# Kernel optimization log

Hardware: AMD Instinct MI355X
Metric: run time of the kernel (lower is better)

Reference implementation:

```python
import jax, jax.numpy as jnp
import numpy as np

EPS = 1e-5
DILATIONS = (1, 2, 4)


def conv2d(x, w, b, pad, groups=1, dil=1):
    # x [B,C,H,W], w [O, C//groups, kh, kw]
    y = jax.lax.conv_general_dilated(
        x, w, window_strides=(1, 1),
        padding=[(pad[0], pad[0]), (pad[1], pad[1])],
        rhs_dilation=(dil, dil),
        dimension_numbers=('NCHW', 'OIHW', 'NCHW'),
        feature_group_count=groups)
    return y + b[None, :, None, None]


def bn(x, p):
    # inference BatchNorm2d; p rows = gamma, beta, mean, var
    g, b, m, v = p[0], p[1], p[2], p[3]
    scale = g * jax.lax.rsqrt(v + EPS)
    return x * scale[None, :, None, None] + (b - m * scale)[None, :, None, None]


def bilinear_sample(img, yy, xx):
    # img [C,H,W]; yy,xx [K,H,W] float sampling coords; zero outside -> [C,K,H,W]
    H, W = img.shape[1], img.shape[2]
    y0f = jnp.floor(yy); x0f = jnp.floor(xx)
    wy1 = yy - y0f; wy0 = 1.0 - wy1
    wx1 = xx - x0f; wx0 = 1.0 - wx1

    def gather(yi, xi):
        valid = (yi >= 0) & (yi < H) & (xi >= 0) & (xi < W)
        yc = jnp.clip(yi, 0, H - 1).astype(jnp.int32)
        xc = jnp.clip(xi, 0, W - 1).astype(jnp.int32)
        v = img[:, yc, xc]  # [C,K,H,W]
        return v * valid.astype(img.dtype)

    y1f = y0f + 1.0; x1f = x0f + 1.0
    return (gather(y0f, x0f) * (wy0 * wx0) + gather(y0f, x1f) * (wy0 * wx1)
            + gather(y1f, x0f) * (wy1 * wx0) + gather(y1f, x1f) * (wy1 * wx1))


def deform_depthwise(x, off, weight, dil):
    # torchvision DeformConv2d, groups=C, kernel 3x3, stride 1, pad=dil, no bias.
    # x [B,C,H,W], off [B,18,H,W] (per-kernel-point (dy,dx)), weight [C,3,3]
    B, C, H, W = x.shape
    off = off.reshape(B, 9, 2, H, W)
    hh = jnp.arange(H, dtype=x.dtype)[:, None]
    ww = jnp.arange(W, dtype=x.dtype)[None, :]
    k = jnp.arange(3, dtype=x.dtype) - 1.0
    ky = jnp.repeat(k, 3)  # [9] row offsets
    kx = jnp.tile(k, 3)    # [9] col offsets
    w9 = weight.reshape(C, 9)

    def per_batch(xb, offb):
        yy = offb[:, 0] + hh[None] + (ky * dil)[:, None, None]  # [9,H,W]
        xx = offb[:, 1] + ww[None] + (kx * dil)[:, None, None]
        s = bilinear_sample(xb, yy, xx)  # [C,9,H,W]
        return jnp.einsum('ckhw,ck->chw', s, w9)

    return jax.vmap(per_batch)(x, off)


def setup_inputs() -> dict:
    key = jax.random.key(0)
    ks = jax.random.split(key, 20)
    B, C, H, W = 2, 64, 192, 192
    r = jax.random.normal
    u = lambda k, s: jax.random.uniform(k, s, minval=0.5, maxval=1.5)
    return {
        'x': r(ks[0], (B, C, H, W)),
        'w_off1': r(ks[1], (C, 1, 1, 15)) * 0.1, 'b_off1': r(ks[2], (C,)) * 0.1,
        'bn_off1': u(ks[3], (4, C)),
        'w_off2': r(ks[4], (C, 1, 15, 1)) * 0.1, 'b_off2': r(ks[5], (C,)) * 0.1,
        'bn_off2': u(ks[6], (4, C)),
        'w_off3': r(ks[7], (C, 1, 3, 3)) * 0.1, 'b_off3': r(ks[8], (C,)) * 0.1,
        'bn_off3': u(ks[9], (4, C)),
        'w_bal_off': r(ks[10], (18, C, 1, 1)) * 0.1, 'b_bal_off': r(ks[11], (18,)) * 0.1,
        'bn_bal_off': u(ks[12], (4, 18)),
        'w_def': r(ks[13], (3, C, 3, 3)) * 0.1,
        'w_bal': r(ks[14], (C, C, 1, 1)) * 0.1, 'b_bal': r(ks[15], (C,)) * 0.1,
        'bn_bal': u(ks[16], (4, C)),
    }


def reference(x, w_off1, b_off1, bn_off1, w_off2, b_off2, bn_off2,
              w_off3, b_off3, bn_off3, w_bal_off, b_bal_off, bn_bal_off,
              w_def, w_bal, b_bal, bn_bal):
    C = x.shape[1]
    # DirectionOffsets: three depthwise conv+BN branches summed, then 1x1 conv+BN -> 18ch
    off_sum = (bn(conv2d(x, w_off1, b_off1, (0, 7), groups=C), bn_off1)
               + bn(conv2d(x, w_off2, b_off2, (7, 0), groups=C), bn_off2)
               + bn(conv2d(x, w_off3, b_off3, (1, 1), groups=C), bn_off3))
    offsets = bn(conv2d(off_sum, w_bal_off, b_bal_off, (0, 0)), bn_bal_off)  # [B,18,H,W]
    # sum of depthwise deformable conv branches (shared offsets, different dilation)
    deform_sum = sum(deform_depthwise(x, offsets, w_def[i], float(d))
                     for i, d in enumerate(DILATIONS))
    # final balance (1x1 conv + BN) gated by x
    return bn(conv2d(deform_sum, w_bal, b_bal, (0, 0)), bn_bal) * x
```

## Files before the change

### kernel.cpp

```cpp
#include <hip/hip_runtime.h>
#include <stdint.h>

constexpr int B = 2, C = 64, H = 192, W = 192;
constexpr int HW = H * W;
constexpr int P = B * H * W;
constexpr float EPS = 1e-5f;

__device__ __forceinline__ int swz(int bid, int nwg) {
  return (bid & 7) * (nwg >> 3) + (bid >> 3);
}

__global__ __launch_bounds__(256) void k_prepw(const float* __restrict__ w1,
    const float* __restrict__ w2, const float* __restrict__ w3,
    const float* __restrict__ wdef, float* __restrict__ w1t,
    float* __restrict__ w2t, float* __restrict__ w3t, float* __restrict__ wdeft) {
  int gid = blockIdx.x * 256 + threadIdx.x;
  const int stride = 8 * 256;
  for (int i = gid; i < 960; i += stride) {
    int c = i & 63, j = i >> 6;
    w1t[i] = w1[c * 15 + j];
    w2t[i] = w2[c * 15 + j];
  }
  for (int i = gid; i < 576; i += stride) {
    int c = i & 63, j = i >> 6;
    w3t[i] = w3[c * 9 + j];
  }
  for (int i = gid; i < 1728; i += stride) {
    int c = i & 63, jk = i >> 6;
    int di = jk / 9, k = jk % 9;
    wdeft[i] = wdef[di * (C * 9) + c * 9 + k];
  }
}

__global__ __launch_bounds__(256) void k_transpose(const float* __restrict__ x,
                                                   float* __restrict__ xt) {
  int blk = swz(blockIdx.x, B * H * (W / 64));
  int wt  = blk % (W / 64);
  int h   = (blk / (W / 64)) % H;
  int b   = blk / ((W / 64) * H);
  int w0  = wt * 64;
  __shared__ float tile[64][65];
  int tx = threadIdx.x & 63;
  int ty = threadIdx.x >> 6;
  #pragma unroll
  for (int c = ty; c < 64; c += 4)
    tile[c][tx] = x[((b * C + c) * H + h) * W + w0 + tx];
  __syncthreads();
  #pragma unroll
  for (int wi = ty; wi < 64; wi += 4)
    xt[((b * H + h) * W + w0 + wi) * 64 + tx] = tile[tx][wi];
}

__global__ __launch_bounds__(256) void k_offsum(const float* __restrict__ xt,
    const float* __restrict__ w1t, const float* __restrict__ b1, const float* __restrict__ bn1,
    const float* __restrict__ w2t, const float* __restrict__ b2, const float* __restrict__ bn2,
    const float* __restrict__ w3t, const float* __restrict__ b3, const float* __restrict__ bn3,
    float* __restrict__ out) {
  int wave = (swz(blockIdx.x, P / 16) * 256 + (int)threadIdx.x) >> 6;
  int c = threadIdx.x & 63;
  int w0 = (wave % (W / 4)) * 4;
  int h  = (wave / (W / 4)) % H;
  int b  = wave / ((W / 4) * H);
  const float* xb = xt + (size_t)b * HW * 64 + c;

  float s1[4] = {0.f, 0.f, 0.f, 0.f};
  float s2[4] = {0.f, 0.f, 0.f, 0.f};
  float s3[4] = {0.f, 0.f, 0.f, 0.f};

  {
    float xv[18];
    #pragma unroll
    for (int j = 0; j < 18; ++j) {
      int ww = w0 - 7 + j;
      xv[j] = (ww >= 0 && ww < W) ? xb[(h * W + ww) * 64] : 0.f;
    }
    #pragma unroll
    for (int j = 0; j < 15; ++j) {
      float wj = w1t[j * 64 + c];
      #pragma unroll
      for (int p = 0; p < 4; ++p) s1[p] = fmaf(xv[p + j], wj, s1[p]);
    }
  }
  #pragma unroll
  for (int j = 0; j < 15; ++j) {
    int hh = h - 7 + j;
    if (hh >= 0 && hh < H) {
      float wj = w2t[j * 64 + c];
      #pragma unroll
      for (int p = 0; p < 4; ++p)
        s2[p] = fmaf(xb[(hh * W + w0 + p) * 64], wj, s2[p]);
    }
  }
  #pragma unroll
  for (int dy = -1; dy <= 1; ++dy) {
    int hh = h + dy;
    if (hh < 0 || hh >= H) continue;
    float rv[6];
    #pragma unroll
    for (int j = 0; j < 6; ++j) {
      int ww = w0 - 1 + j;
      rv[j] = (ww >= 0 && ww < W) ? xb[(hh * W + ww) * 64] : 0.f;
    }
    #pragma unroll
    for (int dx = 0; dx < 3; ++dx) {
      float wj = w3t[((dy + 1) * 3 + dx) * 64 + c];
      #pragma unroll
      for (int p = 0; p < 4; ++p) s3[p] = fmaf(rv[p + dx], wj, s3[p]);
    }
  }

  float sc1 = bn1[c] / sqrtf(bn1[192 + c] + EPS);
  float sh1 = bn1[64 + c] - bn1[128 + c] * sc1;
  float sc2 = bn2[c] / sqrtf(bn2[192 + c] + EPS);
  float sh2 = bn2[64 + c] - bn2[128 + c] * sc2;
  float sc3 = bn3[c] / sqrtf(bn3[192 + c] + EPS);
  float sh3 = bn3[64 + c] - bn3[128 + c] * sc3;
  float bb1 = b1[c], bb2 = b2[c], bb3 = b3[c];
  #pragma unroll
  for (int p = 0; p < 4; ++p)
    out[((size_t)wave * 4 + p) * 64 + c] =
        fmaf(s1[p] + bb1, sc1, sh1) + fmaf(s2[p] + bb2, sc2, sh2) +
        fmaf(s3[p] + bb3, sc3, sh3);
}

__global__ __launch_bounds__(256) void k_offsets(const float* __restrict__ off_sum,
    const float* __restrict__ wq, const float* __restrict__ bq,
    const float* __restrict__ bnq, float* __restrict__ out) {
  int idx = swz(blockIdx.x, (P * 18) / 256) * 256 + (int)threadIdx.x;
  int o   = idx % 18;
  int pix = idx / 18;
  const float4* v  = (const float4*)(off_sum + (size_t)pix * 64);
  const float4* wv = (const float4*)(wq + o * 64);
  float s = 0.f;
  #pragma unroll
  for (int j = 0; j < 16; ++j) {
    float4 a = v[j], ww = wv[j];
    s = fmaf(a.x, ww.x, s); s = fmaf(a.y, ww.y, s);
    s = fmaf(a.z, ww.z, s); s = fmaf(a.w, ww.w, s);
  }
  float sc = bnq[o] / sqrtf(bnq[54 + o] + EPS);
  float sh = bnq[18 + o] - bnq[36 + o] * sc;
  out[idx] = fmaf(s + bq[o], sc, sh);
}

__global__ __launch_bounds__(256) void k_deform(const float* __restrict__ xt,
                                                const float* __restrict__ offs,
                                                const float* __restrict__ wdeft,
                                                float* __restrict__ dsum) {
  __shared__ uint32_t lpre[4][27 * 8 + 4];
  int wl   = threadIdx.x >> 6;
  int lane = threadIdx.x & 63;
  int pix  = swz(blockIdx.x, P / 4) * 4 + wl;

  if (lane < 27) {
    int di = lane / 9, k = lane % 9;
    int d  = 1 << di;
    int w = pix % W, h = (pix / W) % H;
    float offy = offs[(size_t)pix * 18 + 2 * k];
    float offx = offs[(size_t)pix * 18 + 2 * k + 1];
    int ky = k / 3 - 1, kx = k % 3 - 1;
    float yy = (offy + (float)h) + (float)(ky * d);
    float xx = (offx + (float)w) + (float)(kx * d);
    float y0f = floorf(yy), x0f = floorf(xx);
    float wy1 = yy - y0f, wx1 = xx - x0f;
    float wy0 = 1.f - wy1, wx0 = 1.f - wx1;
    int y0 = (int)fmaxf(fminf(y0f, 1.0e4f), -1.0e4f);
    int x0 = (int)fmaxf(fminf(x0f, 1.0e4f), -1.0e4f);
    int y1 = y0 + 1, x1 = x0 + 1;
    float my0 = (y0 >= 0 && y0 < H) ? 1.f : 0.f;
    float my1 = (y1 >= 0 && y1 < H) ? 1.f : 0.f;
    float mx0 = (x0 >= 0 && x0 < W) ? 1.f : 0.f;
    float mx1 = (x1 >= 0 && x1 < W) ? 1.f : 0.f;
    int y0c = min(max(y0, 0), H - 1), y1c = min(max(y1, 0), H - 1);
    int x0c = min(max(x0, 0), W - 1), x1c = min(max(x1, 0), W - 1);
    uint32_t packed = (uint32_t)y0c | ((uint32_t)y1c << 8) |
                      ((uint32_t)x0c << 16) | ((uint32_t)x1c << 24);
    float wy0m = wy0 * my0, wy1m = wy1 * my1;
    float wx0m = wx0 * mx0, wx1m = wx1 * mx1;
    uint32_t* q = &lpre[wl][lane * 8];
    q[0] = packed;
    q[1] = __float_as_uint(wy0m * wx0m);
    q[2] = __float_as_uint(wy0m * wx1m);
    q[3] = __float_as_uint(wy1m * wx0m);
    q[4] = __float_as_uint(wy1m * wx1m);
  }
  __syncthreads();

  int c = lane;
  int b = pix / HW;
  const float* xb = xt + (size_t)b * HW * 64 + c;

  float wd[27];
  #pragma unroll
  for (int i = 0; i < 27; ++i) wd[i] = wdeft[i * 64 + c];

  float acc = 0.f;
  #pragma unroll
  for (int t = 0; t < 27; ++t) {
    uint4 m = *(const uint4*)&lpre[wl][t * 8];
    float w11 = __uint_as_float(lpre[wl][t * 8 + 4]);
    uint32_t pk = m.x;
    float w00 = __uint_as_float(m.y);
    float w01 = __uint_as_float(m.z);
    float w10 = __uint_as_float(m.w);
    int y0 = pk & 255, y1 = (pk >> 8) & 255;
    int x0 = (pk >> 16) & 255, x1 = pk >> 24;
    int r0 = y0 * W, r1 = y1 * W;
    float v00 = xb[(size_t)(r0 + x0) * 64];
    float v01 = xb[(size_t)(r0 + x1) * 64];
    float v10 = xb[(size_t)(r1 + x0) * 64];
    float v11 = xb[(size_t)(r1 + x1) * 64];
    float bil = fmaf(v11, w11, fmaf(v10, w10, fmaf(v01, w01, v00 * w00)));
    acc = fmaf(wd[t], bil, acc);
  }
  dsum[(size_t)pix * 64 + c] = acc;
}

__global__ __launch_bounds__(256) void k_final(const float* __restrict__ ds,
    const float* __restrict__ x, const float* __restrict__ wb,
    const float* __restrict__ bb, const float* __restrict__ bnb,
    float* __restrict__ out) {
  int blk = swz(blockIdx.x, P / 64);
  int w0 = (blk % (W / 64)) * 64;
  int h  = (blk / (W / 64)) % H;
  int b  = blk / ((W / 64) * H);
  __shared__ float dtile[64][68];
  __shared__ float scs[64], shb[64];
  int tx = threadIdx.x & 63;
  int ty = threadIdx.x >> 6;
  int pixbase = (b * H + h) * W + w0;

  {
    int pr  = threadIdx.x >> 4;
    int ic4 = (threadIdx.x & 15) * 4;
    #pragma unroll
    for (int pass = 0; pass < 4; ++pass) {
      int pix = pass * 16 + pr;
      float4 v = *(const float4*)&ds[(size_t)(pixbase + pix) * 64 + ic4];
      *(float4*)&dtile[pix][ic4] = v;
    }
  }
  if (threadIdx.x < 64) {
    float g = bnb[threadIdx.x], vv = bnb[192 + threadIdx.x];
    float sc = g / sqrtf(vv + EPS);
    scs[threadIdx.x] = sc;
    shb[threadIdx.x] = fmaf(bb[threadIdx.x], sc,
                            bnb[64 + threadIdx.x] - bnb[128 + threadIdx.x] * sc);
  }
  __syncthreads();

  float dreg[64];
  #pragma unroll
  for (int q = 0; q < 16; ++q) {
    float4 v = *(float4*)&dtile[tx][q * 4];
    dreg[4 * q + 0] = v.x; dreg[4 * q + 1] = v.y;
    dreg[4 * q + 2] = v.z; dreg[4 * q + 3] = v.w;
  }

  int ocb = __builtin_amdgcn_readfirstlane(ty);
  #pragma unroll
  for (int j = 0; j < 16; ++j) {
    int oc = ocb + 4 * j;
    const float* wr = wb + oc * 64;
    float a0 = 0.f, a1 = 0.f, a2 = 0.f, a3 = 0.f;
    #pragma unroll
    for (int q = 0; q < 16; ++q) {
      a0 = fmaf(dreg[4 * q + 0], wr[4 * q + 0], a0);
      a1 = fmaf(dreg[4 * q + 1], wr[4 * q + 1], a1);
      a2 = fmaf(dreg[4 * q + 2], wr[4 * q + 2], a2);
      a3 = fmaf(dreg[4 * q + 3], wr[4 * q + 3], a3);
    }
    float s = (a0 + a1) + (a2 + a3);
    float val = fmaf(s, scs[oc], shb[oc]);
    int xi = ((b * C + oc) * H + h) * W + w0 + tx;
    out[xi] = val * x[xi];
  }
}

extern "C" void kernel_launch(void* const* d_in, const int* in_sizes, int n_in,
                              void* d_out, int out_size, void* d_ws, size_t ws_size,
                              hipStream_t stream) {
  const float* x     = (const float*)d_in[0];
  const float* w1    = (const float*)d_in[1];
  const float* b1    = (const float*)d_in[2];
  const float* bn1   = (const float*)d_in[3];
  const float* w2    = (const float*)d_in[4];
  const float* b2    = (const float*)d_in[5];
  const float* bn2   = (const float*)d_in[6];
  const float* w3    = (const float*)d_in[7];
  const float* b3    = (const float*)d_in[8];
  const float* bn3   = (const float*)d_in[9];
  const float* wbo   = (const float*)d_in[10];
  const float* bbo   = (const float*)d_in[11];
  const float* bnbo  = (const float*)d_in[12];
  const float* wdef  = (const float*)d_in[13];
  const float* wbal  = (const float*)d_in[14];
  const float* bbal  = (const float*)d_in[15];
  const float* bnbal = (const float*)d_in[16];
  float* out = (float*)d_out;

  float*    xt      = (float*)d_ws;
  float*    off_sum = xt + (size_t)P * 64;
  float*    offs    = off_sum + (size_t)P * 64;
  float*    wts     = offs + (size_t)P * 18;
  float*    w1t     = wts;
  float*    w2t     = wts + 960;
  float*    w3t     = wts + 1920;
  float*    wdeft   = wts + 2496;
  float*    dsum    = off_sum;

  k_prepw<<<8, 256, 0, stream>>>(w1, w2, w3, wdef, w1t, w2t, w3t, wdeft);
  k_transpose<<<B * H * (W / 64), 256, 0, stream>>>(x, xt);
  k_offsum<<<P / 16, 256, 0, stream>>>(xt, w1t, b1, bn1, w2t, b2, bn2, w3t, b3, bn3, off_sum);
  k_offsets<<<(P * 18) / 256, 256, 0, stream>>>(off_sum, wbo, bbo, bnbo, offs);
  k_deform<<<P / 4, 256, 0, stream>>>(xt, offs, wdeft, dsum);
  k_final<<<P / 64, 256, 0, stream>>>(dsum, x, wbal, bbal, bnbal, out);
}
```

Measured before the change: 291.2 us.

## Fuse offset-sum and 1x1 offset conv; precompute byte offsets with scalar addressing in deform

Merges the depthwise offset-sum kernel and the 18-channel 1x1 offset projection into one kernel. The per-pixel 64-channel sums now stay in shared memory and the projection weights are staged there, so the off_sum intermediate is never written to or read back from global memory. In the deform kernel, the four bilinear corner addresses are precomputed as byte offsets in LDS and read with readfirstlane, which makes them wave-uniform scalar bases and removes per-lane unpacking and multiplies. The cost is a 64-float register array per thread in the fused kernel, which may lower occupancy.

```diff
diff --git a/kernel.cpp b/kernel.cpp
--- a/kernel.cpp
+++ b/kernel.cpp
@@ -51,22 +51,37 @@
     xt[((b * H + h) * W + w0 + wi) * 64 + tx] = tile[tx][wi];
 }
 
-__global__ __launch_bounds__(256) void k_offsum(const float* __restrict__ xt,
+__global__ __launch_bounds__(256) void k_offpipe(const float* __restrict__ xt,
     const float* __restrict__ w1t, const float* __restrict__ b1, const float* __restrict__ bn1,
     const float* __restrict__ w2t, const float* __restrict__ b2, const float* __restrict__ bn2,
     const float* __restrict__ w3t, const float* __restrict__ b3, const float* __restrict__ bn3,
-    float* __restrict__ out) {
-  int wave = (swz(blockIdx.x, P / 16) * 256 + (int)threadIdx.x) >> 6;
-  int c = threadIdx.x & 63;
-  int w0 = (wave % (W / 4)) * 4;
-  int h  = (wave / (W / 4)) % H;
-  int b  = wave / ((W / 4) * H);
+    const float* __restrict__ wq, const float* __restrict__ bq, const float* __restrict__ bnq,
+    float* __restrict__ offs) {
+  __shared__ float os[16][68];
+  __shared__ float wqs[18][66];
+  __shared__ float qsc[18], qsh[18];
+
+  int blk = swz(blockIdx.x, P / 16);
+  int w0t = (blk % (W / 16)) * 16;
+  int h   = (blk / (W / 16)) % H;
+  int b   = blk / ((W / 16) * H);
+  int wl  = threadIdx.x >> 6;
+  int c   = threadIdx.x & 63;
+  int w0  = w0t + wl * 4;
   const float* xb = xt + (size_t)b * HW * 64 + c;
+
+  for (int i = threadIdx.x; i < 18 * 64; i += 256)
+    wqs[i >> 6][i & 63] = wq[i];
+  if (threadIdx.x < 18) {
+    int o = threadIdx.x;
+    float sc = bnq[o] / sqrtf(bnq[54 + o] + EPS);
+    qsc[o] = sc;
+    qsh[o] = fmaf(bq[o], sc, bnq[18 + o] - bnq[36 + o] * sc);
+  }
 
   float s1[4] = {0.f, 0.f, 0.f, 0.f};
   float s2[4] = {0.f, 0.f, 0.f, 0.f};
   float s3[4] = {0.f, 0.f, 0.f, 0.f};
-
   {
     float xv[18];
     #pragma unroll
@@ -94,21 +109,21 @@
   #pragma unroll
   for (int dy = -1; dy <= 1; ++dy) {
     int hh = h + dy;
-    if (hh < 0 || hh >= H) continue;
-    float rv[6];
-    #pragma unroll
-    for (int j = 0; j < 6; ++j) {
-      int ww = w0 - 1 + j;
-      rv[j] = (ww >= 0 && ww < W) ? xb[(hh * W + ww) * 64] : 0.f;
-    }
-    #pragma unroll
-    for (int dx = 0; dx < 3; ++dx) {
-      float wj = w3t[((dy + 1) * 3 + dx) * 64 + c];
+    if (hh >= 0 && hh < H) {
+      float rv[6];
       #pragma unroll
-      for (int p = 0; p < 4; ++p) s3[p] = fmaf(rv[p + dx], wj, s3[p]);
-    }
-  }
-
+      for (int j = 0; j < 6; ++j) {
+        int ww = w0 - 1 + j;
+        rv[j] = (ww >= 0 && ww < W) ? xb[(hh * W + ww) * 64] : 0.f;
+      }
+      #pragma unroll
+      for (int dx = 0; dx < 3; ++dx) {
+        float wj = w3t[((dy + 1) * 3 + dx) * 64 + c];
+        #pragma unroll
+        for (int p = 0; p < 4; ++p) s3[p] = fmaf(rv[p + dx], wj, s3[p]);
+      }
+    }
+  }
   float sc1 = bn1[c] / sqrtf(bn1[192 + c] + EPS);
   float sh1 = bn1[64 + c] - bn1[128 + c] * sc1;
   float sc2 = bn2[c] / sqrtf(bn2[192 + c] + EPS);
@@ -118,29 +133,37 @@
   float bb1 = b1[c], bb2 = b2[c], bb3 = b3[c];
   #pragma unroll
   for (int p = 0; p < 4; ++p)
-    out[((size_t)wave * 4 + p) * 64 + c] =
+    os[wl * 4 + p][c] =
         fmaf(s1[p] + bb1, sc1, sh1) + fmaf(s2[p] + bb2, sc2, sh2) +
         fmaf(s3[p] + bb3, sc3, sh3);
-}
-
-__global__ __launch_bounds__(256) void k_offsets(const float* __restrict__ off_sum,
-    const float* __restrict__ wq, const float* __restrict__ bq,
-    const float* __restrict__ bnq, float* __restrict__ out) {
-  int idx = swz(blockIdx.x, (P * 18) / 256) * 256 + (int)threadIdx.x;
-  int o   = idx % 18;
-  int pix = idx / 18;
-  const float4* v  = (const float4*)(off_sum + (size_t)pix * 64);
-  const float4* wv = (const float4*)(wq + o * 64);
-  float s = 0.f;
-  #pragma unroll
-  for (int j = 0; j < 16; ++j) {
-    float4 a = v[j], ww = wv[j];
-    s = fmaf(a.x, ww.x, s); s = fmaf(a.y, ww.y, s);
-    s = fmaf(a.z, ww.z, s); s = fmaf(a.w, ww.w, s);
-  }
-  float sc = bnq[o] / sqrtf(bnq[54 + o] + EPS);
-  float sh = bnq[18 + o] - bnq[36 + o] * sc;
-  out[idx] = fmaf(s + bq[o], sc, sh);
+  __syncthreads();
+
+  int p  = threadIdx.x & 15;
+  int og = threadIdx.x >> 4;
+  float dreg[64];
+  #pragma unroll
+  for (int q = 0; q < 16; ++q) {
+    float4 v = *(float4*)&os[p][q * 4];
+    dreg[4 * q + 0] = v.x; dreg[4 * q + 1] = v.y;
+    dreg[4 * q + 2] = v.z; dreg[4 * q + 3] = v.w;
+  }
+  size_t pix = (size_t)((b * H + h) * W + w0t + p);
+  #pragma unroll
+  for (int pass = 0; pass < 2; ++pass) {
+    int o = (pass == 0) ? og : 16 + og;
+    if (pass == 1 && og >= 2) break;
+    float a0 = 0.f, a1 = 0.f, a2 = 0.f, a3 = 0.f;
+    #pragma unroll
+    for (int q = 0; q < 16; ++q) {
+      float4 ww = *(float4*)&wqs[o][q * 4];
+      a0 = fmaf(dreg[4 * q + 0], ww.x, a0);
+      a1 = fmaf(dreg[4 * q + 1], ww.y, a1);
+      a2 = fmaf(dreg[4 * q + 2], ww.z, a2);
+      a3 = fmaf(dreg[4 * q + 3], ww.w, a3);
+    }
+    float s = (a0 + a1) + (a2 + a3);
+    offs[pix * 18 + o] = fmaf(s, qsc[o], qsh[o]);
+  }
 }
 
 __global__ __launch_bounds__(256) void k_deform(const float* __restrict__ xt,
@@ -173,22 +196,24 @@
     float mx1 = (x1 >= 0 && x1 < W) ? 1.f : 0.f;
     int y0c = min(max(y0, 0), H - 1), y1c = min(max(y1, 0), H - 1);
     int x0c = min(max(x0, 0), W - 1), x1c = min(max(x1, 0), W - 1);
-    uint32_t packed = (uint32_t)y0c | ((uint32_t)y1c << 8) |
-                      ((uint32_t)x0c << 16) | ((uint32_t)x1c << 24);
+    int r0 = y0c * W, r1 = y1c * W;
     float wy0m = wy0 * my0, wy1m = wy1 * my1;
     float wx0m = wx0 * mx0, wx1m = wx1 * mx1;
     uint32_t* q = &lpre[wl][lane * 8];
-    q[0] = packed;
-    q[1] = __float_as_uint(wy0m * wx0m);
-    q[2] = __float_as_uint(wy0m * wx1m);
-    q[3] = __float_as_uint(wy1m * wx0m);
-    q[4] = __float_as_uint(wy1m * wx1m);
+    q[0] = (uint32_t)(r0 + x0c) << 8;
+    q[1] = (uint32_t)(r0 + x1c) << 8;
+    q[2] = (uint32_t)(r1 + x0c) << 8;
+    q[3] = (uint32_t)(r1 + x1c) << 8;
+    q[4] = __float_as_uint(wy0m * wx0m);
+    q[5] = __float_as_uint(wy0m * wx1m);
+    q[6] = __float_as_uint(wy1m * wx0m);
+    q[7] = __float_as_uint(wy1m * wx1m);
   }
   __syncthreads();
 
   int c = lane;
   int b = pix / HW;
-  const float* xb = xt + (size_t)b * HW * 64 + c;
+  const char* xb0 = (const char*)(xt + (size_t)b * HW * 64);
 
   float wd[27];
   #pragma unroll
@@ -197,20 +222,21 @@
   float acc = 0.f;
   #pragma unroll
   for (int t = 0; t < 27; ++t) {
-    uint4 m = *(const uint4*)&lpre[wl][t * 8];
-    float w11 = __uint_as_float(lpre[wl][t * 8 + 4]);
-    uint32_t pk = m.x;
-    float w00 = __uint_as_float(m.y);
-    float w01 = __uint_as_float(m.z);
-    float w10 = __uint_as_float(m.w);
-    int y0 = pk & 255, y1 = (pk >> 8) & 255;
-    int x0 = (pk >> 16) & 255, x1 = pk >> 24;
-    int r0 = y0 * W, r1 = y1 * W;
-    float v00 = xb[(size_t)(r0 + x0) * 64];
-    float v01 = xb[(size_t)(r0 + x1) * 64];
-    float v10 = xb[(size_t)(r1 + x0) * 64];
-    float v11 = xb[(size_t)(r1 + x1) * 64];
-    float bil = fmaf(v11, w11, fmaf(v10, w10, fmaf(v01, w01, v00 * w00)));
+    uint4 ov = *(const uint4*)&lpre[wl][t * 8];
+    uint4 wv = *(const uint4*)&lpre[wl][t * 8 + 4];
+    int s00 = __builtin_amdgcn_readfirstlane((int)ov.x);
+    int s01 = __builtin_amdgcn_readfirstlane((int)ov.y);
+    int s10 = __builtin_amdgcn_readfirstlane((int)ov.z);
+    int s11 = __builtin_amdgcn_readfirstlane((int)ov.w);
+    const float* p00 = (const float*)(xb0 + s00);
+    const float* p01 = (const float*)(xb0 + s01);
+    const float* p10 = (const float*)(xb0 + s10);
+    const float* p11 = (const float*)(xb0 + s11);
+    float v00 = p00[c], v01 = p01[c], v10 = p10[c], v11 = p11[c];
+    float bil = fmaf(v11, __uint_as_float(wv.w),
+                 fmaf(v10, __uint_as_float(wv.z),
+                  fmaf(v01, __uint_as_float(wv.y),
+                       v00 * __uint_as_float(wv.x))));
     acc = fmaf(wd[t], bil, acc);
   }
   dsum[(size_t)pix * 64 + c] = acc;
@@ -299,20 +325,19 @@
   const float* bnbal = (const float*)d_in[16];
   float* out = (float*)d_out;
 
-  float*    xt      = (float*)d_ws;
-  float*    off_sum = xt + (size_t)P * 64;
-  float*    offs    = off_sum + (size_t)P * 64;
-  float*    wts     = offs + (size_t)P * 18;
-  float*    w1t     = wts;
-  float*    w2t     = wts + 960;
-  float*    w3t     = wts + 1920;
-  float*    wdeft   = wts + 2496;
-  float*    dsum    = off_sum;
+  float* xt    = (float*)d_ws;
+  float* dsum  = xt + (size_t)P * 64;
+  float* offs  = dsum + (size_t)P * 64;
+  float* wts   = offs + (size_t)P * 18;
+  float* w1t   = wts;
+  float* w2t   = wts + 960;
+  float* w3t   = wts + 1920;
+  float* wdeft = wts + 2496;
 
   k_prepw<<<8, 256, 0, stream>>>(w1, w2, w3, wdef, w1t, w2t, w3t, wdeft);
   k_transpose<<<B * H * (W / 64), 256, 0, stream>>>(x, xt);
-  k_offsum<<<P / 16, 256, 0, stream>>>(xt, w1t, b1, bn1, w2t, b2, bn2, w3t, b3, bn3, off_sum);
-  k_offsets<<<(P * 18) / 256, 256, 0, stream>>>(off_sum, wbo, bbo, bnbo, offs);
+  k_offpipe<<<P / 16, 256, 0, stream>>>(xt, w1t, b1, bn1, w2t, b2, bn2,
+                                        w3t, b3, bn3, wbo, bbo, bnbo, offs);
   k_deform<<<P / 4, 256, 0, stream>>>(xt, offs, wdeft, dsum);
   k_final<<<P / 64, 256, 0, stream>>>(dsum, x, wbal, bbal, bnbal, out);
 }
```

Result: faster. 244.7 us (-16.0%).
